# Performance work log

Measured on AMD Instinct MI355X. Metric: run time of the kernel, lower is better.

Reference implementation:

```python
import jax, jax.numpy as jnp
import numpy as np

K = 5          # kernel_size per dim
B = 100        # batch size (hard-coded in source)
GRID = 28
NUM_FIRST_FC = 49  # adjs[2].size(0) = 7*7


def spline_conv(x, edge_index, pseudo, W, root, bias):
    """Degree-1 open B-spline graph conv (SplineGCN).
    x: [N, Cin]; edge_index: [2, E] (src, dst); pseudo: [E, 2] in [0,1];
    W: [K*K, Cin, Cout]; root: [Cin, Cout]; bias: [Cout].
    out_i = mean_{j->i} sum_taps b_tap(u_ij) * (x_j @ W[k_tap]) + x_i @ root + bias
    """
    N = x.shape[0]
    src, dst = edge_index[0], edge_index[1]
    pos = pseudo * (K - 1)                     # open spline: scale to [0, K-1]
    kf = jnp.floor(pos)
    frac = pos - kf                            # [E, 2]
    k0 = kf.astype(jnp.int32)
    k1 = jnp.minimum(k0 + 1, K - 1)
    # Precompute x @ W[k] for all 25 kernel indices: [N, K*K, Cout]
    y = jnp.einsum('ni,kio->nko', x, W)
    fx, fy = frac[:, 0], frac[:, 1]
    taps = [
        (k0[:, 0], k0[:, 1], (1 - fx) * (1 - fy)),
        (k0[:, 0], k1[:, 1], (1 - fx) * fy),
        (k1[:, 0], k0[:, 1], fx * (1 - fy)),
        (k1[:, 0], k1[:, 1], fx * fy),
    ]
    msg = jnp.zeros((src.shape[0], W.shape[2]), dtype=x.dtype)
    for ax, ay, w in taps:
        msg = msg + w[:, None] * y[src, ax * K + ay]   # gather [E, Cout]
    agg = jax.ops.segment_sum(msg, dst, num_segments=N)
    deg = jax.ops.segment_sum(jnp.ones_like(msg[:, 0]), dst, num_segments=N)
    return agg / jnp.maximum(deg, 1.0)[:, None] + x @ root + bias


def max_pool2(x):  # x: [b, H, W, C] -> [b, H/2, W/2, C] (same math as NCHW pool)
    b, h, w, c = x.shape
    return x.reshape(b, h // 2, 2, w // 2, 2, c).max(axis=(2, 4))


def setup_inputs() -> dict:
    key = jax.random.key(0)
    ks = jax.random.split(key, 16)
    N0, N1 = B * GRID * GRID, B * (GRID // 2) * (GRID // 2)
    E0, E1 = N0 * 8, N1 * 8
    s = 0.1
    return {
        'x': jax.random.normal(ks[0], (N0, 1), dtype=jnp.float32),
        'pseudo0': jax.random.uniform(ks[1], (E0, 2), dtype=jnp.float32),
        'pseudo1': jax.random.uniform(ks[2], (E1, 2), dtype=jnp.float32),
        'W1': jax.random.normal(ks[3], (K * K, 1, 32), dtype=jnp.float32) * s,
        'root1': jax.random.normal(ks[4], (1, 32), dtype=jnp.float32) * s,
        'b1': jnp.zeros((32,), dtype=jnp.float32),
        'W2': jax.random.normal(ks[5], (K * K, 32, 64), dtype=jnp.float32) * s,
        'root2': jax.random.normal(ks[6], (32, 64), dtype=jnp.float32) * s,
        'b2': jnp.zeros((64,), dtype=jnp.float32),
        'fc1_w': jax.random.normal(ks[7], (NUM_FIRST_FC * 64, 512), dtype=jnp.float32) * 0.02,
        'fc1_b': jnp.zeros((512,), dtype=jnp.float32),
        'fc2_w': jax.random.normal(ks[8], (512, 10), dtype=jnp.float32) * 0.02,
        'fc2_b': jnp.zeros((10,), dtype=jnp.float32),
        'edge_index0': jax.random.randint(ks[9], (2, E0), 0, N0, dtype=jnp.int32),
        'edge_index1': jax.random.randint(ks[10], (2, E1), 0, N1, dtype=jnp.int32),
    }


def reference(x, pseudo0, pseudo1, W1, root1, b1, W2, root2, b2,
              fc1_w, fc1_b, fc2_w, fc2_b, edge_index0, edge_index1):
    elu = jax.nn.elu
    # conv1 on 28x28 grid graph
    h = elu(spline_conv(x, edge_index0, pseudo0, W1, root1, b1))   # [B*784, 32]
    h = h.reshape(-1, GRID, GRID, 32)                              # [B, 28, 28, 32]
    h = max_pool2(h)                                               # [B, 14, 14, 32]
    h = h.reshape(-1, 32)                                          # [B*196, 32]
    # conv2 on 14x14 grid graph
    h = elu(spline_conv(h, edge_index1, pseudo1, W2, root2, b2))   # [B*196, 64]
    # faithful replication of the source's reshapes: (B*196) rows -> (B/4, 28, 28, 64)
    h = h.reshape(-1, GRID, GRID, 64)                              # [25, 28, 28, 64]
    h = max_pool2(h)                                               # [25, 14, 14, 64]
    h = h.reshape(-1, NUM_FIRST_FC * 64)                           # [100, 3136]
    h = elu(h @ fc1_w + fc1_b)
    # F.dropout with training=False (eval) is identity
    h = elu(h @ fc2_w + fc2_b)
    return jax.nn.log_softmax(h, axis=-1)
```

## Files before the change

kernel.cpp:

```cpp
#include <hip/hip_runtime.h>
#include <hip/hip_bf16.h>

#define KK 5
constexpr int N0 = 78400;
constexpr int E0 = 627200;
constexpr int N1 = 19600;
constexpr int E1 = 156800;
constexpr int C1 = 32, C2 = 64;
constexpr int BSZ = 100;
constexpr int FC1_IN = 3136, FC1_OUT = 512;
constexpr int NKEYS = 98000;
constexpr int NCOARSE = 383;
constexpr int CAPB = 2400;
constexpr int KEXT = 832;
constexpr int ULS = 836;
constexpr int UBS = 856;
constexpr int CH2 = 160;
constexpr int CH1 = 640;
constexpr int KZ = 7;

typedef __attribute__((ext_vector_type(8))) short bf16x8;
typedef __attribute__((ext_vector_type(4))) float f32x4;

__device__ __forceinline__ unsigned short f2bf(float f) {
    union { float f; unsigned u; } v; v.f = f;
    unsigned u = v.u;
    unsigned r = (u + 0x7FFF + ((u >> 16) & 1)) >> 16;
    return (unsigned short)r;
}

__device__ __forceinline__ void taps4(float px, float py,
                                      int& a00, int& a01, int& a10, int& a11,
                                      float& fx, float& fy) {
    float kfx = floorf(px), kfy = floorf(py);
    fx = px - kfx; fy = py - kfy;
    int k0x = min(max((int)kfx, 0), KK - 1);
    int k0y = min(max((int)kfy, 0), KK - 1);
    int k1x = min(k0x + 1, KK - 1), k1y = min(k0y + 1, KK - 1);
    a00 = k0x * KK + k0y; a01 = k0x * KK + k1y;
    a10 = k1x * KK + k0y; a11 = k1x * KK + k1y;
}

__global__ void coarse_bin(const int* __restrict__ ei0, const int* __restrict__ ei1,
                           const float* __restrict__ ps0, const float* __restrict__ ps1,
                           int* __restrict__ gcur, int2* __restrict__ pk2,
                           const float* __restrict__ fc1w, const float* __restrict__ W2,
                           const float* __restrict__ root2,
                           unsigned short* __restrict__ wt1,
                           unsigned short* __restrict__ w2t) {
    __shared__ int hist[NCOARSE];
    __shared__ int gbase[NCOARSE];
    __shared__ unsigned short tile[64 * 66];
    int t = threadIdx.x;
    if (blockIdx.x >= 192) {
        int pb = blockIdx.x - 192;
        if (pb >= 392) {
            int base = (pb - 392) * 6656;
            for (int i2 = t; i2 < 6656; i2 += 512) {
                int idx = base + i2;
                int o = idx / KEXT, k = idx - o * KEXT;
                float v = (k < 800) ? W2[k * 64 + o] : root2[(k - 800) * 64 + o];
                w2t[idx] = f2bf(v);
            }
            return;
        }
        int k0 = (pb >> 3) * 64, j0 = (pb & 7) * 64;
        int jj = t & 63, ks = t >> 6;
        for (int kk = ks; kk < 64; kk += 8)
            tile[kk * 66 + jj] = f2bf(fc1w[(k0 + kk) * FC1_OUT + j0 + jj]);
        __syncthreads();
        int kk2 = t & 63, js = t >> 6;
        for (int j2 = js; j2 < 64; j2 += 8)
            wt1[(j0 + j2) * FC1_IN + k0 + kk2] = tile[kk2 * 66 + j2];
        return;
    }
    for (int i = t; i < NCOARSE; i += 512) hist[i] = 0;
    __syncthreads();
    int e0b = blockIdx.x * 4096;
    int keys[8], rnk[8], pay0[8], pay1[8];
#pragma unroll
    for (int j = 0; j < 8; j++) {
        int e = e0b + t + j * 512;
        int gk = -1, p0 = 0, p1v = 0;
        if (e < E0) {
            gk = ei0[E0 + e];
            float px = ps0[2 * e] * 4.f, py = ps0[2 * e + 1] * 4.f;
            unsigned ux = min((unsigned)(px * 16384.f + 0.5f), 65535u);
            unsigned uy = min((unsigned)(py * 16384.f + 0.5f), 65535u);
            p0 = ei0[e]; p1v = (int)(ux | (uy << 16));
        } else if (e < E0 + E1) {
            int el = e - E0;
            gk = N0 + ei1[E1 + el];
            float px = ps1[2 * el] * 4.f, py = ps1[2 * el + 1] * 4.f;
            unsigned ux = min((unsigned)(px * 16384.f + 0.5f), 65535u);
            unsigned uy = min((unsigned)(py * 16384.f + 0.5f), 65535u);
            p0 = ei1[el]; p1v = (int)(ux | (uy << 16));
        }
        keys[j] = gk; pay0[j] = p0; pay1[j] = p1v;
    }
#pragma unroll
    for (int j = 0; j < 8; j++)
        if (keys[j] >= 0) rnk[j] = atomicAdd(&hist[keys[j] >> 8], 1);
    __syncthreads();
    for (int i = t; i < NCOARSE; i += 512)
        gbase[i] = hist[i] ? atomicAdd(&gcur[i], hist[i]) : 0;
    __syncthreads();
#pragma unroll
    for (int j = 0; j < 8; j++) {
        if (keys[j] >= 0) {
            int b = keys[j] >> 8;
            int p = gbase[b] + rnk[j];
            if (p < CAPB)
                pk2[b * CAPB + p] = make_int2(pay0[j] | ((keys[j] & 255) << 20), pay1[j]);
        }
    }
}

__global__ void fine_sort(const int2* __restrict__ pk2, const int* __restrict__ gcur,
                          int2* __restrict__ erec, int* __restrict__ off) {
    __shared__ int cl[NCOARSE];
    __shared__ int2 ent[CAPB];
    __shared__ int rnk[CAPB];
    __shared__ int h2[256];
    __shared__ int sc[256];
    __shared__ int redbuf[4];
    __shared__ int baseS;
    int b = blockIdx.x, t = threadIdx.x;
    for (int i2 = t; i2 < NCOARSE; i2 += 256) cl[i2] = min(gcur[i2], CAPB);
    __syncthreads();
    {
        int s = 0;
        if (t < b) s += cl[t];
        if (t + 256 < b) s += cl[t + 256];
#pragma unroll
        for (int o2 = 32; o2 > 0; o2 >>= 1) s += __shfl_down(s, o2);
        if ((t & 63) == 0) redbuf[t >> 6] = s;
        __syncthreads();
        if (t == 0) baseS = redbuf[0] + redbuf[1] + redbuf[2] + redbuf[3];
        __syncthreads();
    }
    int base = baseS;
    int cb = cl[b];
    h2[t] = 0;
    __syncthreads();
    for (int i = t; i < cb; i += 256) {
        int2 v = pk2[b * CAPB + i];
        ent[i] = v;
        rnk[i] = atomicAdd(&h2[(v.x >> 20) & 255], 1);
    }
    __syncthreads();
    int v0 = h2[t];
    sc[t] = v0;
    __syncthreads();
    for (int d = 1; d < 256; d <<= 1) {
        int add = (t >= d) ? sc[t - d] : 0;
        __syncthreads();
        sc[t] += add;
        __syncthreads();
    }
    int excl = sc[t] - v0;
    __syncthreads();
    sc[t] = excl;
    __syncthreads();
    int n = (b << 8) + t;
    if (n < NKEYS) off[n] = base + excl;
    if (b == 0 && t == 0) off[NKEYS] = E0 + E1;
    for (int i = t; i < cb; i += 256) {
        int2 v = ent[i];
        erec[base + sc[(v.x >> 20) & 255] + rnk[i]] = v;
    }
}

__global__ __launch_bounds__(256, 4)
void conv1_pool(const int2* __restrict__ erec, const int* __restrict__ off,
                const float* __restrict__ x,
                const float* __restrict__ W1,
                const float* __restrict__ root, const float* __restrict__ bias,
                float* __restrict__ p1) {
    __shared__ float S4[224 * 25];
    __shared__ float Sr[56 * 25];
    __shared__ float exv[CH1], efx[CH1], efy[CH1];
    __shared__ int   emt[CH1];
    float* h1t = S4;
    int t = threadIdx.x;
    int bb = blockIdx.x;
    int n0 = bb * 56;
    int q = t & 3, nl = t >> 2;
    bool actN = nl < 56;
    int n = n0 + (actN ? nl : 0);
    float* sp = S4 + (actN ? (nl * 4 + q) : 0) * 25;
    for (int i = t; i < 224 * 25; i += 256) S4[i] = 0.f;
    int e0 = off[n0], e1 = off[n0 + 56];
    int my0 = off[n], my1 = off[n + 1];
    for (int base = e0; base < e1; base += CH1) {
        int nE = min(e1 - base, CH1);
        __syncthreads();
        for (int j = t; j < nE; j += 256) {
            int2 r = erec[base + j];
            int src = r.x & 0xFFFFF;
            float px = (float)((unsigned)r.y & 0xFFFF) * (1.f / 16384.f);
            float py = (float)((unsigned)r.y >> 16) * (1.f / 16384.f);
            int a00, a01, a10, a11; float fx, fy;
            taps4(px, py, a00, a01, a10, a11, fx, fy);
            emt[j] = a00 | (a01 << 5) | (a10 << 10) | (a11 << 15);
            efx[j] = fx; efy[j] = fy;
            exv[j] = x[src];
        }
        __syncthreads();
        if (actN) {
            int r0 = max(my0 - base, 0), r1 = min(my1 - base, nE);
            for (int p = r0 + q; p < r1; p += 4) {
                float xv = exv[p]; int m = emt[p];
                float fx = efx[p], fy = efy[p];
                float gx = 1.f - fx, gy = 1.f - fy;
                sp[m & 31]         += gx * gy * xv;
                sp[(m >> 5) & 31]  += gx * fy * xv;
                sp[(m >> 10) & 31] += fx * gy * xv;
                sp[(m >> 15) & 31] += fx * fy * xv;
            }
        }
    }
    __syncthreads();
    for (int i2 = t; i2 < 56 * 25; i2 += 256) {
        int n2 = i2 / 25, a = i2 - n2 * 25;
        Sr[i2] = S4[(n2 * 4 + 0) * 25 + a] + S4[(n2 * 4 + 1) * 25 + a] +
                 S4[(n2 * 4 + 2) * 25 + a] + S4[(n2 * 4 + 3) * 25 + a];
    }
    __syncthreads();
    {
        int o = t & 31, ng = t >> 5;
        float w1c[25];
#pragma unroll
        for (int a = 0; a < 25; a++) w1c[a] = W1[a * C1 + o];
        float ro = root[o], bo = bias[o];
        for (int j2 = 0; j2 < 7; j2++) {
            int nl2 = ng * 7 + j2;
            int n2 = n0 + nl2;
            float acc = 0.f;
#pragma unroll
            for (int a = 0; a < 25; a++) acc += Sr[nl2 * 25 + a] * w1c[a];
            float invd = 1.f / fmaxf((float)(off[n2 + 1] - off[n2]), 1.f);
            float v = acc * invd + x[n2] * ro + bo;
            h1t[nl2 * 32 + o] = v > 0.f ? v : expm1f(v);
        }
    }
    __syncthreads();
    for (int i2 = t; i2 < 448; i2 += 256) {
        int o2 = i2 & 31, pc = i2 >> 5;
        float m0 = h1t[(2 * pc) * 32 + o2],      m1 = h1t[(2 * pc + 1) * 32 + o2];
        float m2 = h1t[(28 + 2 * pc) * 32 + o2], m3 = h1t[(28 + 2 * pc + 1) * 32 + o2];
        p1[(bb * 14 + pc) * C1 + o2] = fmaxf(fmaxf(m0, m1), fmaxf(m2, m3));
    }
}

__global__ __launch_bounds__(512, 4)
void conv2_fused(const float* __restrict__ p1, const int2* __restrict__ erec,
                 const int* __restrict__ off,
                 const unsigned short* __restrict__ w2t,
                 const float* __restrict__ b2, float* __restrict__ h2) {
    __shared__ float Ul[16 * ULS];
    __shared__ float ev[CH2 * 32];
    __shared__ int   es[CH2];
    __shared__ int   et[CH2];
    __shared__ float efx[CH2], efy[CH2];
    unsigned short* Ub = (unsigned short*)Ul;
    int t = threadIdx.x;
    int nb = blockIdx.x * 16;
    int i = t & 31;
    int g = t >> 5;
    float* up = Ul + g * ULS;
#pragma unroll
    for (int a = 0; a < 25; a++) up[a * 32 + i] = 0.f;
    up[800 + i] = p1[(nb + g) * C1 + i];
    int e0 = off[N0 + nb], e1 = off[N0 + nb + 16];
    int my0 = off[N0 + nb + g], my1 = off[N0 + nb + g + 1];
    for (int base = e0; base < e1; base += CH2) {
        int nE = min(e1 - base, CH2);
        __syncthreads();
        for (int j = t; j < nE; j += 512) {
            int2 r = erec[base + j];
            es[j] = r.x & 0xFFFFF;
            float px = (float)((unsigned)r.y & 0xFFFF) * (1.f / 16384.f);
            float py = (float)((unsigned)r.y >> 16) * (1.f / 16384.f);
            int a00, a01, a10, a11; float fx, fy;
            taps4(px, py, a00, a01, a10, a11, fx, fy);
            et[j] = a00 | (a01 << 5) | (a10 << 10) | (a11 << 15);
            efx[j] = fx; efy[j] = fy;
        }
        __syncthreads();
        for (int j0 = g; j0 < nE; j0 += 64) {
            int ja = j0, jb = j0 + 16, jc = j0 + 32, jd = j0 + 48;
            bool vb = jb < nE, vc = jc < nE, vd = jd < nE;
            int sa = es[ja];
            int sb = vb ? es[jb] : sa;
            int sc2 = vc ? es[jc] : sa;
            int sd = vd ? es[jd] : sa;
            float xa = p1[sa * C1 + i];
            float xb = p1[sb * C1 + i];
            float xc = p1[sc2 * C1 + i];
            float xd = p1[sd * C1 + i];
            ev[ja * 32 + i] = xa;
            if (vb) ev[jb * 32 + i] = xb;
            if (vc) ev[jc * 32 + i] = xc;
            if (vd) ev[jd * 32 + i] = xd;
        }
        __syncthreads();
        int r0 = max(my0 - base, 0);
        int r1 = min(my1 - base, nE);
        for (int p = r0; p < r1; p++) {
            float xv = ev[p * 32 + i];
            int m = et[p];
            float fx = efx[p], fy = efy[p];
            float gx = 1.f - fx, gy = 1.f - fy;
            up[(m & 31) * 32 + i]         += gx * gy * xv;
            up[((m >> 5) & 31) * 32 + i]  += gx * fy * xv;
            up[((m >> 10) & 31) * 32 + i] += fx * gy * xv;
            up[((m >> 15) & 31) * 32 + i] += fx * fy * xv;
        }
    }
    __syncthreads();
    {
        int g2 = t >> 5, i2c = t & 31;
        int dgc = off[N0 + nb + g2 + 1] - off[N0 + nb + g2];
        float invd = 1.f / fmaxf((float)dgc, 1.f);
        const float* srcp = Ul + g2 * ULS + i2c * 26;
        float rv[26];
#pragma unroll
        for (int j = 0; j < 26; j++) {
            float v = srcp[j];
            rv[j] = (i2c * 26 + j < 800) ? v * invd : v;
        }
        __syncthreads();
        unsigned* dstp = (unsigned*)(Ub + g2 * UBS + i2c * 26);
#pragma unroll
        for (int j = 0; j < 13; j++) {
            unsigned lo = f2bf(rv[2 * j]), hi = f2bf(rv[2 * j + 1]);
            dstp[j] = lo | (hi << 16);
        }
    }
    __syncthreads();
    int wv = t >> 6, lane = t & 63, quad = lane >> 4, lrow = lane & 15;
    if (wv < 4) {
        f32x4 acc = {0.f, 0.f, 0.f, 0.f};
        const unsigned short* bbase = w2t + (wv * 16 + lrow) * KEXT;
        const unsigned short* abase = Ub + lrow * UBS;
#pragma unroll
        for (int kc = 0; kc < 26; kc++) {
            bf16x8 a = *(const bf16x8*)(abase + kc * 32 + quad * 8);
            bf16x8 b = *(const bf16x8*)(bbase + kc * 32 + quad * 8);
            acc = __builtin_amdgcn_mfma_f32_16x16x32_bf16(a, b, acc, 0, 0, 0);
        }
        int o = wv * 16 + lrow;
        float bo = b2[o];
#pragma unroll
        for (int r = 0; r < 4; r++) {
            int node = quad * 4 + r;
            float v = acc[r] + bo;
            v = v > 0.f ? v : expm1f(v);
            h2[(nb + node) * C2 + o] = v;
        }
    }
}

__global__ void pool2b(const float* __restrict__ h2, unsigned short* __restrict__ p2b) {
    int idx = blockIdx.x * blockDim.x + threadIdx.x;
    if (idx >= 112 * FC1_IN) return;
    if (idx >= 100 * FC1_IN) { p2b[idx] = 0; return; }
    int o = idx & 63; int t2 = idx >> 6;
    int c = t2 % 14; int r = (t2 / 14) % 14; int b = t2 / 196;
    const float* base = h2 + (((b * 28 + 2 * r) * 28 + 2 * c) * C2 + o);
    float m = fmaxf(fmaxf(base[0], base[C2]),
                    fmaxf(base[28 * C2], base[28 * C2 + C2]));
    p2b[idx] = f2bf(m);
}

__global__ void gemm_fc1(const unsigned short* __restrict__ p2b,
                         const unsigned short* __restrict__ wt1,
                         float* __restrict__ z1p) {
    constexpr int AS = 232;
    __shared__ unsigned short as_[16 * AS];
    int t = threadIdx.x;
    int jt = blockIdx.x, mt = blockIdx.y, kz = blockIdx.z;
    int wv = t >> 6, lane = t & 63, quad = lane >> 4, lrow = lane & 15;
    int m0 = mt * 16;
    int kbase = kz * 448;
    const unsigned short* bbase = wt1 + (jt * 64 + wv * 16 + lrow) * FC1_IN + kbase;
    f32x4 acc = {0.f, 0.f, 0.f, 0.f};
    for (int ch = 0; ch < 2; ch++) {
        __syncthreads();
        for (int slot = t; slot < 448; slot += 256) {
            int r = slot / 28, c = slot - (slot / 28) * 28;
            *(uint4*)(as_ + r * AS + c * 8) =
                *(const uint4*)(p2b + (m0 + r) * FC1_IN + kbase + ch * 224 + c * 8);
        }
        __syncthreads();
        const unsigned short* ab = as_ + lrow * AS;
        const unsigned short* bb = bbase + ch * 224;
#pragma unroll
        for (int kk = 0; kk < 7; kk++) {
            bf16x8 a = *(const bf16x8*)(ab + kk * 32 + quad * 8);
            bf16x8 b = *(const bf16x8*)(bb + kk * 32 + quad * 8);
            acc = __builtin_amdgcn_mfma_f32_16x16x32_bf16(a, b, acc, 0, 0, 0);
        }
    }
    int n = jt * 64 + wv * 16 + lrow;
#pragma unroll
    for (int r = 0; r < 4; r++) {
        int m = m0 + quad * 4 + r;
        z1p[kz * (112 * FC1_OUT) + m * FC1_OUT + n] = acc[r];
    }
}

__global__ void fc2_lsm(const float* __restrict__ z1p, const float* __restrict__ fc1b,
                        const float* __restrict__ w, const float* __restrict__ fc2b,
                        float* __restrict__ out) {
    int b = blockIdx.x;
    int t = threadIdx.x;
    int wv = t >> 6;
    int lane = t & 63;
    float acc = 0.f;
#pragma unroll
    for (int m = 0; m < 8; m++) {
        int k = lane * 8 + m;
        float xv = fc1b[k];
#pragma unroll
        for (int p = 0; p < KZ; p++)
            xv += z1p[p * (112 * FC1_OUT) + b * FC1_OUT + k];
        xv = xv > 0.f ? xv : expm1f(xv);
        acc += xv * w[k * 10 + wv];
    }
#pragma unroll
    for (int off = 32; off > 0; off >>= 1) acc += __shfl_down(acc, off);
    __shared__ float zs[10];
    if (lane == 0) {
        float z = acc + fc2b[wv];
        zs[wv] = z > 0.f ? z : expm1f(z);
    }
    __syncthreads();
    if (t < 10) {
        float m = -1e30f;
        for (int jj = 0; jj < 10; jj++) m = fmaxf(m, zs[jj]);
        float s = 0.f;
        for (int jj = 0; jj < 10; jj++) s += expf(zs[jj] - m);
        out[b * 10 + t] = zs[t] - m - logf(s);
    }
}

extern "C" void kernel_launch(void* const* d_in, const int* in_sizes, int n_in,
                              void* d_out, int out_size, void* d_ws, size_t ws_size,
                              hipStream_t stream) {
    const float* x     = (const float*)d_in[0];
    const float* ps0   = (const float*)d_in[1];
    const float* ps1   = (const float*)d_in[2];
    const float* W1    = (const float*)d_in[3];
    const float* root1 = (const float*)d_in[4];
    const float* b1    = (const float*)d_in[5];
    const float* W2    = (const float*)d_in[6];
    const float* root2 = (const float*)d_in[7];
    const float* b2v   = (const float*)d_in[8];
    const float* fc1w  = (const float*)d_in[9];
    const float* fc1b  = (const float*)d_in[10];
    const float* fc2w  = (const float*)d_in[11];
    const float* fc2b  = (const float*)d_in[12];
    const int*   ei0   = (const int*)d_in[13];
    const int*   ei1   = (const int*)d_in[14];

    float* ws = (float*)d_ws;
    int*  gcur = (int*)ws;
    int*  off  = (int*)(ws + 384);
    int2* pk2  = (int2*)(ws + 98388);
    int2* erec = (int2*)(ws + 1936788);
    float* p1  = ws + 3504788;
    float* h2  = ws + 4131988;
    unsigned short* p2b = (unsigned short*)(ws + 5386388);
    float* z1p = ws + 5562004;
    unsigned short* w2t = (unsigned short*)(ws + 5963412);
    unsigned short* wt1 = (unsigned short*)(ws + 5990036);

    hipMemsetAsync(gcur, 0, (size_t)NCOARSE * sizeof(int), stream);

    coarse_bin<<<592, 512, 0, stream>>>(ei0, ei1, ps0, ps1, gcur, pk2,
                                        fc1w, W2, root2, wt1, w2t);
    fine_sort<<<NCOARSE, 256, 0, stream>>>(pk2, gcur, erec, off);
    conv1_pool<<<1400, 256, 0, stream>>>(erec, off, x, W1, root1, b1, p1);
    conv2_fused<<<N1 / 16, 512, 0, stream>>>(p1, erec, off, w2t, b2v, h2);
    pool2b<<<(112 * FC1_IN + 255) / 256, 256, 0, stream>>>(h2, p2b);
    gemm_fc1<<<dim3(8, 7, KZ), 256, 0, stream>>>(p2b, wt1, z1p);
    fc2_lsm<<<BSZ, 640, 0, stream>>>(z1p, fc1b, fc2w, fc2b, (float*)d_out);
}
```

Baseline: 203.4 us.

## Bin edges directly by consumer block and accumulate with fixed-point LDS atomics

Removes the fine_sort kernel and CSR offsets. coarse_bin now buckets edges by the exact conv1 or conv2 block that consumes them, and the conv kernels read their bucket directly. They scatter into shared memory with integer atomics on fixed-point scaled values, and degrees are counted in the same pass. This drops one kernel launch and a global sort pass. In exchange it adds LDS atomic contention, fixed-point rounding error, and fixed per-bucket capacities that silently drop edges if a bucket overflows.

```diff
diff --git a/kernel.cpp b/kernel.cpp
--- a/kernel.cpp
+++ b/kernel.cpp
@@ -9,15 +9,21 @@
 constexpr int C1 = 32, C2 = 64;
 constexpr int BSZ = 100;
 constexpr int FC1_IN = 3136, FC1_OUT = 512;
-constexpr int NKEYS = 98000;
-constexpr int NCOARSE = 383;
-constexpr int CAPB = 2400;
 constexpr int KEXT = 832;
 constexpr int ULS = 836;
 constexpr int UBS = 856;
-constexpr int CH2 = 160;
-constexpr int CH1 = 640;
 constexpr int KZ = 7;
+
+constexpr int NB0 = 1400;
+constexpr int CAP0 = 576;
+constexpr int NB1 = 1225;
+constexpr int CAP1 = 224;
+constexpr int NBT = NB0 + NB1;
+
+constexpr float SC1  = 4194304.f;
+constexpr float ISC1 = 1.f / 4194304.f;
+constexpr float SC2  = 1048576.f;
+constexpr float ISC2 = 1.f / 1048576.f;
 
 typedef __attribute__((ext_vector_type(8))) short bf16x8;
 typedef __attribute__((ext_vector_type(4))) float f32x4;
@@ -43,13 +49,14 @@
 
 __global__ void coarse_bin(const int* __restrict__ ei0, const int* __restrict__ ei1,
                            const float* __restrict__ ps0, const float* __restrict__ ps1,
-                           int* __restrict__ gcur, int2* __restrict__ pk2,
+                           int* __restrict__ gcur,
+                           int2* __restrict__ pk0, int2* __restrict__ pk1,
                            const float* __restrict__ fc1w, const float* __restrict__ W2,
                            const float* __restrict__ root2,
                            unsigned short* __restrict__ wt1,
                            unsigned short* __restrict__ w2t) {
-    __shared__ int hist[NCOARSE];
-    __shared__ int gbase[NCOARSE];
+    __shared__ int hist[NBT];
+    __shared__ int gbase[NBT];
     __shared__ unsigned short tile[64 * 66];
     int t = threadIdx.x;
     if (blockIdx.x >= 192) {
@@ -74,157 +81,84 @@
             wt1[(j0 + j2) * FC1_IN + k0 + kk2] = tile[kk2 * 66 + j2];
         return;
     }
-    for (int i = t; i < NCOARSE; i += 512) hist[i] = 0;
+    for (int i = t; i < NBT; i += 512) hist[i] = 0;
     __syncthreads();
     int e0b = blockIdx.x * 4096;
     int keys[8], rnk[8], pay0[8], pay1[8];
 #pragma unroll
     for (int j = 0; j < 8; j++) {
         int e = e0b + t + j * 512;
-        int gk = -1, p0 = 0, p1v = 0;
+        int k = -1, p0 = 0, p1v = 0;
         if (e < E0) {
-            gk = ei0[E0 + e];
+            int dst = ei0[E0 + e];
+            int b = dst / 56, low = dst - b * 56;
+            k = b;
             float px = ps0[2 * e] * 4.f, py = ps0[2 * e + 1] * 4.f;
             unsigned ux = min((unsigned)(px * 16384.f + 0.5f), 65535u);
             unsigned uy = min((unsigned)(py * 16384.f + 0.5f), 65535u);
-            p0 = ei0[e]; p1v = (int)(ux | (uy << 16));
+            p0 = ei0[e] | (low << 20); p1v = (int)(ux | (uy << 16));
         } else if (e < E0 + E1) {
             int el = e - E0;
-            gk = N0 + ei1[E1 + el];
+            int dst = ei1[E1 + el];
+            k = NB0 + (dst >> 4);
             float px = ps1[2 * el] * 4.f, py = ps1[2 * el + 1] * 4.f;
             unsigned ux = min((unsigned)(px * 16384.f + 0.5f), 65535u);
             unsigned uy = min((unsigned)(py * 16384.f + 0.5f), 65535u);
-            p0 = ei1[el]; p1v = (int)(ux | (uy << 16));
-        }
-        keys[j] = gk; pay0[j] = p0; pay1[j] = p1v;
+            p0 = ei1[el] | ((dst & 15) << 20); p1v = (int)(ux | (uy << 16));
+        }
+        keys[j] = k; pay0[j] = p0; pay1[j] = p1v;
     }
 #pragma unroll
     for (int j = 0; j < 8; j++)
-        if (keys[j] >= 0) rnk[j] = atomicAdd(&hist[keys[j] >> 8], 1);
-    __syncthreads();
-    for (int i = t; i < NCOARSE; i += 512)
+        if (keys[j] >= 0) rnk[j] = atomicAdd(&hist[keys[j]], 1);
+    __syncthreads();
+    for (int i = t; i < NBT; i += 512)
         gbase[i] = hist[i] ? atomicAdd(&gcur[i], hist[i]) : 0;
     __syncthreads();
 #pragma unroll
     for (int j = 0; j < 8; j++) {
         if (keys[j] >= 0) {
-            int b = keys[j] >> 8;
-            int p = gbase[b] + rnk[j];
-            if (p < CAPB)
-                pk2[b * CAPB + p] = make_int2(pay0[j] | ((keys[j] & 255) << 20), pay1[j]);
-        }
-    }
-}
-
-__global__ void fine_sort(const int2* __restrict__ pk2, const int* __restrict__ gcur,
-                          int2* __restrict__ erec, int* __restrict__ off) {
-    __shared__ int cl[NCOARSE];
-    __shared__ int2 ent[CAPB];
-    __shared__ int rnk[CAPB];
-    __shared__ int h2[256];
-    __shared__ int sc[256];
-    __shared__ int redbuf[4];
-    __shared__ int baseS;
-    int b = blockIdx.x, t = threadIdx.x;
-    for (int i2 = t; i2 < NCOARSE; i2 += 256) cl[i2] = min(gcur[i2], CAPB);
-    __syncthreads();
-    {
-        int s = 0;
-        if (t < b) s += cl[t];
-        if (t + 256 < b) s += cl[t + 256];
-#pragma unroll
-        for (int o2 = 32; o2 > 0; o2 >>= 1) s += __shfl_down(s, o2);
-        if ((t & 63) == 0) redbuf[t >> 6] = s;
-        __syncthreads();
-        if (t == 0) baseS = redbuf[0] + redbuf[1] + redbuf[2] + redbuf[3];
-        __syncthreads();
-    }
-    int base = baseS;
-    int cb = cl[b];
-    h2[t] = 0;
-    __syncthreads();
-    for (int i = t; i < cb; i += 256) {
-        int2 v = pk2[b * CAPB + i];
-        ent[i] = v;
-        rnk[i] = atomicAdd(&h2[(v.x >> 20) & 255], 1);
-    }
-    __syncthreads();
-    int v0 = h2[t];
-    sc[t] = v0;
-    __syncthreads();
-    for (int d = 1; d < 256; d <<= 1) {
-        int add = (t >= d) ? sc[t - d] : 0;
-        __syncthreads();
-        sc[t] += add;
-        __syncthreads();
-    }
-    int excl = sc[t] - v0;
-    __syncthreads();
-    sc[t] = excl;
-    __syncthreads();
-    int n = (b << 8) + t;
-    if (n < NKEYS) off[n] = base + excl;
-    if (b == 0 && t == 0) off[NKEYS] = E0 + E1;
-    for (int i = t; i < cb; i += 256) {
-        int2 v = ent[i];
-        erec[base + sc[(v.x >> 20) & 255] + rnk[i]] = v;
+            int k = keys[j];
+            int p = gbase[k] + rnk[j];
+            if (k < NB0) {
+                if (p < CAP0) pk0[k * CAP0 + p] = make_int2(pay0[j], pay1[j]);
+            } else {
+                if (p < CAP1) pk1[(k - NB0) * CAP1 + p] = make_int2(pay0[j], pay1[j]);
+            }
+        }
     }
 }
 
 __global__ __launch_bounds__(256, 4)
-void conv1_pool(const int2* __restrict__ erec, const int* __restrict__ off,
+void conv1_pool(const int2* __restrict__ pk0, const int* __restrict__ cnt0,
                 const float* __restrict__ x,
                 const float* __restrict__ W1,
                 const float* __restrict__ root, const float* __restrict__ bias,
                 float* __restrict__ p1) {
-    __shared__ float S4[224 * 25];
-    __shared__ float Sr[56 * 25];
-    __shared__ float exv[CH1], efx[CH1], efy[CH1];
-    __shared__ int   emt[CH1];
-    float* h1t = S4;
+    __shared__ int   Ui[56 * 26];
+    __shared__ float h1t[56 * 32];
     int t = threadIdx.x;
     int bb = blockIdx.x;
     int n0 = bb * 56;
-    int q = t & 3, nl = t >> 2;
-    bool actN = nl < 56;
-    int n = n0 + (actN ? nl : 0);
-    float* sp = S4 + (actN ? (nl * 4 + q) : 0) * 25;
-    for (int i = t; i < 224 * 25; i += 256) S4[i] = 0.f;
-    int e0 = off[n0], e1 = off[n0 + 56];
-    int my0 = off[n], my1 = off[n + 1];
-    for (int base = e0; base < e1; base += CH1) {
-        int nE = min(e1 - base, CH1);
-        __syncthreads();
-        for (int j = t; j < nE; j += 256) {
-            int2 r = erec[base + j];
-            int src = r.x & 0xFFFFF;
-            float px = (float)((unsigned)r.y & 0xFFFF) * (1.f / 16384.f);
-            float py = (float)((unsigned)r.y >> 16) * (1.f / 16384.f);
-            int a00, a01, a10, a11; float fx, fy;
-            taps4(px, py, a00, a01, a10, a11, fx, fy);
-            emt[j] = a00 | (a01 << 5) | (a10 << 10) | (a11 << 15);
-            efx[j] = fx; efy[j] = fy;
-            exv[j] = x[src];
-        }
-        __syncthreads();
-        if (actN) {
-            int r0 = max(my0 - base, 0), r1 = min(my1 - base, nE);
-            for (int p = r0 + q; p < r1; p += 4) {
-                float xv = exv[p]; int m = emt[p];
-                float fx = efx[p], fy = efy[p];
-                float gx = 1.f - fx, gy = 1.f - fy;
-                sp[m & 31]         += gx * gy * xv;
-                sp[(m >> 5) & 31]  += gx * fy * xv;
-                sp[(m >> 10) & 31] += fx * gy * xv;
-                sp[(m >> 15) & 31] += fx * fy * xv;
-            }
-        }
-    }
-    __syncthreads();
-    for (int i2 = t; i2 < 56 * 25; i2 += 256) {
-        int n2 = i2 / 25, a = i2 - n2 * 25;
-        Sr[i2] = S4[(n2 * 4 + 0) * 25 + a] + S4[(n2 * 4 + 1) * 25 + a] +
-                 S4[(n2 * 4 + 2) * 25 + a] + S4[(n2 * 4 + 3) * 25 + a];
+    for (int i = t; i < 56 * 26; i += 256) Ui[i] = 0;
+    __syncthreads();
+    int cnt = min(cnt0[bb], CAP0);
+    const int2* bkt = pk0 + bb * CAP0;
+    for (int j = t; j < cnt; j += 256) {
+        int2 r = bkt[j];
+        int src = r.x & 0xFFFFF, low = (r.x >> 20) & 63;
+        float px = (float)((unsigned)r.y & 0xFFFF) * (1.f / 16384.f);
+        float py = (float)((unsigned)r.y >> 16) * (1.f / 16384.f);
+        int a00, a01, a10, a11; float fx, fy;
+        taps4(px, py, a00, a01, a10, a11, fx, fy);
+        float xv = x[src];
+        float gx = 1.f - fx, gy = 1.f - fy;
+        int* row = Ui + low * 26;
+        atomicAdd(row + a00, __float2int_rn(gx * gy * xv * SC1));
+        atomicAdd(row + a01, __float2int_rn(gx * fy * xv * SC1));
+        atomicAdd(row + a10, __float2int_rn(fx * gy * xv * SC1));
+        atomicAdd(row + a11, __float2int_rn(fx * fy * xv * SC1));
+        atomicAdd(row + 25, 1);
     }
     __syncthreads();
     {
@@ -234,14 +168,14 @@
         for (int a = 0; a < 25; a++) w1c[a] = W1[a * C1 + o];
         float ro = root[o], bo = bias[o];
         for (int j2 = 0; j2 < 7; j2++) {
-            int nl2 = ng * 7 + j2;
-            int n2 = n0 + nl2;
+            int nl = ng * 7 + j2;
+            int n = n0 + nl;
             float acc = 0.f;
 #pragma unroll
-            for (int a = 0; a < 25; a++) acc += Sr[nl2 * 25 + a] * w1c[a];
-            float invd = 1.f / fmaxf((float)(off[n2 + 1] - off[n2]), 1.f);
-            float v = acc * invd + x[n2] * ro + bo;
-            h1t[nl2 * 32 + o] = v > 0.f ? v : expm1f(v);
+            for (int a = 0; a < 25; a++) acc += (float)Ui[nl * 26 + a] * w1c[a];
+            float invd = ISC1 / fmaxf((float)Ui[nl * 26 + 25], 1.f);
+            float v = acc * invd + x[n] * ro + bo;
+            h1t[nl * 32 + o] = v > 0.f ? v : expm1f(v);
         }
     }
     __syncthreads();
@@ -253,82 +187,64 @@
     }
 }
 
-__global__ __launch_bounds__(512, 4)
-void conv2_fused(const float* __restrict__ p1, const int2* __restrict__ erec,
-                 const int* __restrict__ off,
+__global__ __launch_bounds__(512, 2)
+void conv2_fused(const float* __restrict__ p1, const int2* __restrict__ pk1,
+                 const int* __restrict__ cnt1,
                  const unsigned short* __restrict__ w2t,
                  const float* __restrict__ b2, float* __restrict__ h2) {
-    __shared__ float Ul[16 * ULS];
-    __shared__ float ev[CH2 * 32];
-    __shared__ int   es[CH2];
-    __shared__ int   et[CH2];
-    __shared__ float efx[CH2], efy[CH2];
-    unsigned short* Ub = (unsigned short*)Ul;
+    __shared__ int   Ui[16 * ULS];
+    __shared__ int   es[CAP1];
+    __shared__ int   et[CAP1];
+    __shared__ float efx[CAP1], efy[CAP1];
+    __shared__ int   degc[16];
+    unsigned short* Ub = (unsigned short*)Ui;
     int t = threadIdx.x;
-    int nb = blockIdx.x * 16;
+    int bx = blockIdx.x;
+    int nb = bx * 16;
     int i = t & 31;
     int g = t >> 5;
-    float* up = Ul + g * ULS;
-#pragma unroll
-    for (int a = 0; a < 25; a++) up[a * 32 + i] = 0.f;
-    up[800 + i] = p1[(nb + g) * C1 + i];
-    int e0 = off[N0 + nb], e1 = off[N0 + nb + 16];
-    int my0 = off[N0 + nb + g], my1 = off[N0 + nb + g + 1];
-    for (int base = e0; base < e1; base += CH2) {
-        int nE = min(e1 - base, CH2);
-        __syncthreads();
-        for (int j = t; j < nE; j += 512) {
-            int2 r = erec[base + j];
-            es[j] = r.x & 0xFFFFF;
-            float px = (float)((unsigned)r.y & 0xFFFF) * (1.f / 16384.f);
-            float py = (float)((unsigned)r.y >> 16) * (1.f / 16384.f);
-            int a00, a01, a10, a11; float fx, fy;
-            taps4(px, py, a00, a01, a10, a11, fx, fy);
-            et[j] = a00 | (a01 << 5) | (a10 << 10) | (a11 << 15);
-            efx[j] = fx; efy[j] = fy;
-        }
-        __syncthreads();
-        for (int j0 = g; j0 < nE; j0 += 64) {
-            int ja = j0, jb = j0 + 16, jc = j0 + 32, jd = j0 + 48;
-            bool vb = jb < nE, vc = jc < nE, vd = jd < nE;
-            int sa = es[ja];
-            int sb = vb ? es[jb] : sa;
-            int sc2 = vc ? es[jc] : sa;
-            int sd = vd ? es[jd] : sa;
-            float xa = p1[sa * C1 + i];
-            float xb = p1[sb * C1 + i];
-            float xc = p1[sc2 * C1 + i];
-            float xd = p1[sd * C1 + i];
-            ev[ja * 32 + i] = xa;
-            if (vb) ev[jb * 32 + i] = xb;
-            if (vc) ev[jc * 32 + i] = xc;
-            if (vd) ev[jd * 32 + i] = xd;
-        }
-        __syncthreads();
-        int r0 = max(my0 - base, 0);
-        int r1 = min(my1 - base, nE);
-        for (int p = r0; p < r1; p++) {
-            float xv = ev[p * 32 + i];
-            int m = et[p];
-            float fx = efx[p], fy = efy[p];
-            float gx = 1.f - fx, gy = 1.f - fy;
-            up[(m & 31) * 32 + i]         += gx * gy * xv;
-            up[((m >> 5) & 31) * 32 + i]  += gx * fy * xv;
-            up[((m >> 10) & 31) * 32 + i] += fx * gy * xv;
-            up[((m >> 15) & 31) * 32 + i] += fx * fy * xv;
-        }
+    int* up = Ui + g * ULS;
+#pragma unroll
+    for (int a = 0; a < 25; a++) up[a * 32 + i] = 0;
+    up[800 + i] = __float2int_rn(p1[(nb + g) * C1 + i] * SC2);
+    if (t < 16) degc[t] = 0;
+    __syncthreads();
+    int cnt = min(cnt1[bx], CAP1);
+    for (int j = t; j < cnt; j += 512) {
+        int2 r = pk1[bx * CAP1 + j];
+        es[j] = r.x;
+        float px = (float)((unsigned)r.y & 0xFFFF) * (1.f / 16384.f);
+        float py = (float)((unsigned)r.y >> 16) * (1.f / 16384.f);
+        int a00, a01, a10, a11; float fx, fy;
+        taps4(px, py, a00, a01, a10, a11, fx, fy);
+        et[j] = a00 | (a01 << 5) | (a10 << 10) | (a11 << 15);
+        efx[j] = fx; efy[j] = fy;
+        atomicAdd(&degc[(r.x >> 20) & 15], 1);
+    }
+    __syncthreads();
+    for (int j = g; j < cnt; j += 16) {
+        int rx = es[j];
+        float xv = p1[(rx & 0xFFFFF) * C1 + i];
+        int* row = Ui + ((rx >> 20) & 15) * ULS;
+        int m = et[j];
+        float fx = efx[j], fy = efy[j];
+        float gx = 1.f - fx, gy = 1.f - fy;
+        atomicAdd(row + (m & 31) * 32 + i,         __float2int_rn(gx * gy * xv * SC2));
+        atomicAdd(row + ((m >> 5) & 31) * 32 + i,  __float2int_rn(gx * fy * xv * SC2));
+        atomicAdd(row + ((m >> 10) & 31) * 32 + i, __float2int_rn(fx * gy * xv * SC2));
+        atomicAdd(row + ((m >> 15) & 31) * 32 + i, __float2int_rn(fx * fy * xv * SC2));
     }
     __syncthreads();
     {
         int g2 = t >> 5, i2c = t & 31;
-        int dgc = off[N0 + nb + g2 + 1] - off[N0 + nb + g2];
-        float invd = 1.f / fmaxf((float)dgc, 1.f);
-        const float* srcp = Ul + g2 * ULS + i2c * 26;
+        float invd = 1.f / fmaxf((float)degc[g2], 1.f);
+        float stap = ISC2 * invd;
+        const int* srcp = Ui + g2 * ULS + i2c * 26;
         float rv[26];
 #pragma unroll
         for (int j = 0; j < 26; j++) {
-            float v = srcp[j];
-            rv[j] = (i2c * 26 + j < 800) ? v * invd : v;
+            float v = (float)srcp[j];
+            rv[j] = (i2c * 26 + j < 800) ? v * stap : v * ISC2;
         }
         __syncthreads();
         unsigned* dstp = (unsigned*)(Ub + g2 * UBS + i2c * 26);
@@ -467,23 +383,21 @@
 
     float* ws = (float*)d_ws;
     int*  gcur = (int*)ws;
-    int*  off  = (int*)(ws + 384);
-    int2* pk2  = (int2*)(ws + 98388);
-    int2* erec = (int2*)(ws + 1936788);
-    float* p1  = ws + 3504788;
-    float* h2  = ws + 4131988;
-    unsigned short* p2b = (unsigned short*)(ws + 5386388);
-    float* z1p = ws + 5562004;
-    unsigned short* w2t = (unsigned short*)(ws + 5963412);
-    unsigned short* wt1 = (unsigned short*)(ws + 5990036);
-
-    hipMemsetAsync(gcur, 0, (size_t)NCOARSE * sizeof(int), stream);
-
-    coarse_bin<<<592, 512, 0, stream>>>(ei0, ei1, ps0, ps1, gcur, pk2,
+    int2* pk0  = (int2*)(ws + 2688);
+    int2* pk1  = (int2*)(ws + 1615488);
+    float* p1  = ws + 2164288;
+    float* h2  = ws + 2791488;
+    unsigned short* p2b = (unsigned short*)(ws + 4045888);
+    float* z1p = ws + 4221504;
+    unsigned short* w2t = (unsigned short*)(ws + 4622912);
+    unsigned short* wt1 = (unsigned short*)(ws + 4649536);
+
+    hipMemsetAsync(gcur, 0, (size_t)NBT * sizeof(int), stream);
+
+    coarse_bin<<<592, 512, 0, stream>>>(ei0, ei1, ps0, ps1, gcur, pk0, pk1,
                                         fc1w, W2, root2, wt1, w2t);
-    fine_sort<<<NCOARSE, 256, 0, stream>>>(pk2, gcur, erec, off);
-    conv1_pool<<<1400, 256, 0, stream>>>(erec, off, x, W1, root1, b1, p1);
-    conv2_fused<<<N1 / 16, 512, 0, stream>>>(p1, erec, off, w2t, b2v, h2);
+    conv1_pool<<<NB0, 256, 0, stream>>>(pk0, gcur, x, W1, root1, b1, p1);
+    conv2_fused<<<NB1, 512, 0, stream>>>(p1, pk1, gcur + NB0, w2t, b2v, h2);
     pool2b<<<(112 * FC1_IN + 255) / 256, 256, 0, stream>>>(h2, p2b);
     gemm_fc1<<<dim3(8, 7, KZ), 256, 0, stream>>>(p2b, wt1, z1p);
     fc2_lsm<<<BSZ, 640, 0, stream>>>(z1p, fc1b, fc2w, fc2b, (float*)d_out);
```

Result: faster. 186.4 us (-8.4%).
